# Kernel tuning notes

Hardware: AMD Instinct MI355X
Metric: run time of the kernel (lower is better)

The kernel has to match this reference:

```python
import jax, jax.numpy as jnp
import numpy as np

B, N, E = 2, 50000, 400000
C_IN, D, C, S, H, L, FFN = 5, 2, 128, 32, 8, 4, 512
COORD_F, TIME_F, FREQ_BASE, BETA = 8, 4, 1000.0, 1.0
HD = C // H


def setup_inputs() -> dict:
    key = jax.random.key(0)
    ks = jax.random.split(key, 32)
    sc = 0.02
    inp = {
        'inputs': jax.random.normal(ks[0], (B, N, C_IN), jnp.float32),
        'coords': jax.random.uniform(ks[1], (B, N, D), jnp.float32),
        't_norm': jax.random.uniform(ks[2], (B,), jnp.float32),
        'adj_indices': jax.random.randint(ks[3], (2, E), 0, N, jnp.int64 if jax.config.jax_enable_x64 else jnp.int32),
        'adj_values': jax.random.uniform(ks[4], (E,), jnp.float32) * 0.25,  # ~1/avg_degree for stable magnitudes
        'freq_matrix': jax.random.normal(ks[5], (D, COORD_F), jnp.float32),
        'embed_W': jax.random.normal(ks[6], (C_IN + 2 * COORD_F + 2 * TIME_F, C), jnp.float32) * sc,
        'embed_b': jnp.zeros((C,), jnp.float32),
        'ln1_g': jnp.ones((L, C), jnp.float32),
        'ln1_b': jnp.zeros((L, C), jnp.float32),
        'Wslice': jax.random.normal(ks[7], (L, C, S), jnp.float32) * sc,
        'bslice': jnp.zeros((L, S), jnp.float32),
        'Wfront': jax.random.normal(ks[8], (L, C, S), jnp.float32) * sc,
        'bfront': jnp.zeros((L, S), jnp.float32),
        'Win': jax.random.normal(ks[9], (L, C, 3 * C), jnp.float32) * sc,
        'b_in': jnp.zeros((L, 3 * C), jnp.float32),
        'Wout': jax.random.normal(ks[10], (L, C, C), jnp.float32) * sc,
        'bout': jnp.zeros((L, C), jnp.float32),
        'ln2_g': jnp.ones((L, C), jnp.float32),
        'ln2_b': jnp.zeros((L, C), jnp.float32),
        'Wff1': jax.random.normal(ks[11], (L, C, FFN), jnp.float32) * sc,
        'bff1': jnp.zeros((L, FFN), jnp.float32),
        'Wff2': jax.random.normal(ks[12], (L, FFN, C), jnp.float32) * sc,
        'bff2': jnp.zeros((L, C), jnp.float32),
        'proj_W': jax.random.normal(ks[13], (C, C_IN), jnp.float32) * sc,
        'proj_b': jnp.zeros((C_IN,), jnp.float32),
    }
    return inp


def _layer_norm(x, g, b, eps=1e-5):
    m = jnp.mean(x, -1, keepdims=True)
    v = jnp.mean(jnp.square(x - m), -1, keepdims=True)
    return (x - m) * jax.lax.rsqrt(v + eps) * g + b


def _forward(inputs, coords, t_norm, adj_indices, adj_values, freq_matrix,
             embed_W, embed_b, ln1_g, ln1_b, Wslice, bslice, Wfront, bfront,
             Win, b_in, Wout, bout, ln2_g, ln2_b, Wff1, bff1, Wff2, bff2,
             proj_W, proj_b):
    rows, cols = adj_indices[0], adj_indices[1]
    b, n = coords.shape[0], coords.shape[1]
    # spatial Fourier encoding (B,N,2*COORD_F)
    p = 2.0 * jnp.pi * (coords @ freq_matrix)
    sp_enc = jnp.concatenate([jnp.sin(p), jnp.cos(p)], -1)
    # temporal encoding (B,N,2*TIME_F)
    omega = FREQ_BASE ** (-jnp.arange(TIME_F, dtype=jnp.float32) / TIME_F)
    ang = omega[None, :] * (t_norm * FREQ_BASE)[:, None]
    t_enc = jnp.broadcast_to(jnp.concatenate([jnp.sin(ang), jnp.cos(ang)], -1)[:, None, :], (b, n, 2 * TIME_F))
    x = jnp.concatenate([inputs, sp_enc, t_enc], -1) @ embed_W + embed_b  # (B,N,C)
    weights_all = []
    for l in range(L):
        h = _layer_norm(x, ln1_g[l], ln1_b[l])
        # sparse adjacency aggregation: y[r] += a_e * h[c] (duplicates sum == coalesce)
        contrib = adj_values[None, :, None] * h[:, cols, :]  # (B,E,C)
        h_local = jax.vmap(lambda cb: jax.ops.segment_sum(cb, rows, num_segments=n))(contrib)
        h_front = h - h_local
        logits = h @ Wslice[l] + bslice[l] + BETA * (h_front @ Wfront[l] + bfront[l])
        w = jax.nn.softmax(logits, -1)  # (B,N,S)
        wsum = jnp.maximum(jnp.sum(w, axis=1)[:, :, None], 1e-8)  # (B,S,1)
        slices = jnp.einsum('bns,bnc->bsc', w, h) / wsum  # (B,S,C)
        # slice-space MHA (self-attention on S tokens)
        qkv = slices @ Win[l] + b_in[l]
        q, k, v = jnp.split(qkv, 3, axis=-1)
        def split_heads(t):
            return t.reshape(b, S, H, HD).transpose(0, 2, 1, 3)  # (B,H,S,HD)
        qh, kh, vh = split_heads(q), split_heads(k), split_heads(v)
        attn = jax.nn.softmax(jnp.einsum('bhqd,bhkd->bhqk', qh, kh) / jnp.sqrt(jnp.float32(HD)), -1)
        o = jnp.einsum('bhqk,bhkd->bhqd', attn, vh).transpose(0, 2, 1, 3).reshape(b, S, C)
        slices_out = o @ Wout[l] + bout[l]
        x = x + jnp.einsum('bns,bsc->bnc', w, slices_out)
        h2 = _layer_norm(x, ln2_g[l], ln2_b[l])
        x = x + jax.nn.gelu(h2 @ Wff1[l] + bff1[l], approximate=False) @ Wff2[l] + bff2[l]
        weights_all.append(w)
    out = x @ proj_W + proj_b  # (B,N,C_OUT)
    return out, jnp.stack(weights_all)  # (L,B,N,S)


def reference(inputs, coords, t_norm, adj_indices, adj_values, freq_matrix,
              embed_W, embed_b, ln1_g, ln1_b, Wslice, bslice, Wfront, bfront,
              Win, b_in, Wout, bout, ln2_g, ln2_b, Wff1, bff1, Wff2, bff2,
              proj_W, proj_b):
    return _forward(inputs, coords, t_norm, adj_indices, adj_values, freq_matrix,
                    embed_W, embed_b, ln1_g, ln1_b, Wslice, bslice, Wfront, bfront,
                    Win, b_in, Wout, bout, ln2_g, ln2_b, Wff1, bff1, Wff2, bff2,
                    proj_W, proj_b)
```

## Files before the change

kernel.cpp:

```cpp
#include <hip/hip_runtime.h>
#include <math.h>

#define BATCH 2
#define NN 50000
#define NE 400000
#define C_IN 5
#define CC 128
#define SS 32
#define NH 8
#define NL 4
#define FFN 512
#define COORD_F 8
#define TIME_F 4
#define HD 16
#define BETA 1.0f
#define TWO_PI 6.283185307179586476925287f

#define NTOT (BATCH * NN)
#define FF_MT 128
#define FF_BLOCKS ((NTOT + FF_MT - 1) / FF_MT)
#define MPAD (FF_BLOCKS * FF_MT)
#define NBLK ((NN + 127) / 128)
#define LP_PAD 136
#define H2S 136
#define HIDS 72

typedef unsigned short u16;
typedef unsigned int u32;
typedef __attribute__((ext_vector_type(8))) __bf16 bf16x8;
typedef __attribute__((ext_vector_type(4))) float f32x4;

__device__ __forceinline__ u16 f2bf(float f) {
    union { __bf16 b; u16 u; } v;
    v.b = (__bf16)f;
    return v.u;
}

__device__ __forceinline__ float bf2f(u16 h) {
    union { u32 u; float f; } v; v.u = ((u32)h) << 16;
    return v.f;
}

__device__ __forceinline__ float gelu_f(float a) {
    float xx = a * 0.7071067811865475f;
    float ax = fabsf(xx);
    float t = 1.0f / fmaf(0.3275911f, ax, 1.0f);
    float poly = t * fmaf(t, fmaf(t, fmaf(t, fmaf(t, 1.061405429f, -1.453152027f),
                                          1.421413741f), -0.284496736f), 0.254829592f);
    float e = __expf(-ax * ax);
    float erfv = copysignf(fmaf(-poly, e, 1.0f), xx);
    return 0.5f * a * (1.0f + erfv);
}

__global__ void count_deg(const int* rows, int* deg) {
    int e = blockIdx.x * blockDim.x + threadIdx.x;
    if (e < NE) atomicAdd(&deg[rows[e]], 1);
}

__global__ __launch_bounds__(512) void scan_deg(const int* deg, int* rowptr) {
    __shared__ int part[512];
    int t = threadIdx.x;
    const int CH = (NN + 511) / 512;
    int begin = t * CH, end = min(begin + CH, NN);
    int s = 0;
    for (int i = begin; i < end; i++) s += deg[i];
    part[t] = s;
    __syncthreads();
    for (int off = 1; off < 512; off <<= 1) {
        int v = (t >= off) ? part[t - off] : 0;
        __syncthreads();
        part[t] += v;
        __syncthreads();
    }
    int base = (t == 0) ? 0 : part[t - 1];
    for (int i = begin; i < end; i++) { rowptr[i] = base; base += deg[i]; }
    if (t == 511) rowptr[NN] = part[511];
}

__global__ void fill_csr(const int* rows, const int* cols, const float* vals,
                         int* cursor, int* csr_col, float* csr_val) {
    int e = blockIdx.x * blockDim.x + threadIdx.x;
    if (e < NE) {
        int p = atomicAdd(&cursor[rows[e]], 1);
        csr_col[p] = cols[e];
        csr_val[p] = vals[e];
    }
}

__global__ __launch_bounds__(128) void embed_ln1_kernel(const float* inputs, const float* coords,
                                                        const float* t_norm, const float* freq,
                                                        const float* W, const float* bias,
                                                        const float* g, const float* bb,
                                                        float* x, u16* hbf) {
    int node = blockIdx.x;
    int b = node / NN;
    int t = threadIdx.x;
    __shared__ float feat[32];
    __shared__ float sm[4];
    if (t < 8) {
        float c0 = coords[node * 2 + 0], c1 = coords[node * 2 + 1];
        float p = TWO_PI * (c0 * freq[t] + c1 * freq[8 + t]);
        feat[5 + t] = sinf(p);
        feat[13 + t] = cosf(p);
    } else if (t < 12) {
        int j = t - 8;
        float omega = powf(1000.0f, -(float)j * 0.25f);
        float ang = omega * t_norm[b] * 1000.0f;
        feat[21 + j] = sinf(ang);
        feat[25 + j] = cosf(ang);
    } else if (t >= 16 && t < 21) {
        feat[t - 16] = inputs[node * 5 + (t - 16)];
    }
    __syncthreads();
    float acc = bias[t];
    #pragma unroll
    for (int k = 0; k < 29; k++) acc += feat[k] * W[k * CC + t];
    x[(size_t)node * CC + t] = acc;
    float s = acc;
    #pragma unroll
    for (int off = 32; off > 0; off >>= 1) s += __shfl_xor(s, off, 64);
    if ((t & 63) == 0) sm[t >> 6] = s;
    __syncthreads();
    float mean = (sm[0] + sm[1]) * (1.0f / 128.0f);
    float d = acc - mean;
    float ss = d * d;
    #pragma unroll
    for (int off = 32; off > 0; off >>= 1) ss += __shfl_xor(ss, off, 64);
    if ((t & 63) == 0) sm[2 + (t >> 6)] = ss;
    __syncthreads();
    float var = (sm[2] + sm[3]) * (1.0f / 128.0f);
    hbf[(size_t)node * CC + t] = f2bf(d * rsqrtf(var + 1e-5f) * g[t] + bb[t]);
}

__global__ __launch_bounds__(128) void agg_kernel(const u16* hbf, const int* rowptr,
                                                  const int* csr_col, const float* csr_val,
                                                  u16* hlbf) {
    int blk = blockIdx.x;
    int b = blk / NN, r = blk % NN;
    int t = threadIdx.x;
    int s0 = rowptr[r], s1 = rowptr[r + 1];
    const u16* hb = hbf + (size_t)b * NN * CC;
    float a0 = 0.0f, a1 = 0.0f, a2 = 0.0f, a3 = 0.0f;
    int e = s0;
    for (; e + 4 <= s1; e += 4) {
        int c0 = csr_col[e], c1 = csr_col[e + 1], c2 = csr_col[e + 2], c3 = csr_col[e + 3];
        float v0 = csr_val[e], v1 = csr_val[e + 1], v2 = csr_val[e + 2], v3 = csr_val[e + 3];
        u16 h0 = hb[(size_t)c0 * CC + t];
        u16 h1 = hb[(size_t)c1 * CC + t];
        u16 h2 = hb[(size_t)c2 * CC + t];
        u16 h3 = hb[(size_t)c3 * CC + t];
        a0 += v0 * bf2f(h0);
        a1 += v1 * bf2f(h1);
        a2 += v2 * bf2f(h2);
        a3 += v3 * bf2f(h3);
    }
    for (; e < s1; e++) a0 += csr_val[e] * bf2f(hb[(size_t)csr_col[e] * CC + t]);
    hlbf[(size_t)blk * CC + t] = f2bf((a0 + a1) + (a2 + a3));
}

__global__ __launch_bounds__(256) void pack_logits_weights(const float* Ws, const float* bs,
                                                           const float* Wf, const float* bf,
                                                           u16* Wcombp, float* bcombp) {
    int idx = blockIdx.x * 256 + threadIdx.x;
    if (idx >= NL * SS * 256) return;
    int l = idx / (SS * 256);
    int r = idx - l * (SS * 256);
    int s = r >> 8, k = r & 255;
    float v;
    if (k < 128)
        v = Ws[(size_t)l * CC * SS + (size_t)k * SS + s] + BETA * Wf[(size_t)l * CC * SS + (size_t)k * SS + s];
    else
        v = -BETA * Wf[(size_t)l * CC * SS + (size_t)(k - 128) * SS + s];
    Wcombp[idx] = f2bf(v);
    if (k == 0) bcombp[l * SS + s] = bs[l * SS + s] + BETA * bf[l * SS + s];
}

__global__ __launch_bounds__(256, 2) void logits_pool(const u16* __restrict__ hbf,
                                                      const u16* __restrict__ hlbf,
                                                      const u16* __restrict__ Wcomb,
                                                      const float* __restrict__ bcomb,
                                                      float* __restrict__ wout,
                                                      u16* __restrict__ whi,
                                                      u16* __restrict__ wlo,
                                                      float* __restrict__ slices_acc,
                                                      float* __restrict__ wsum) {
    __shared__ __align__(16) u16 hT[128 * LP_PAD];
    __shared__ __align__(16) u16 wTh[SS * LP_PAD];
    __shared__ __align__(16) u16 wTl[SS * LP_PAD];
    __shared__ float wsum_sh[SS];
    int t = threadIdx.x;
    int b = blockIdx.y;
    int nl0 = blockIdx.x * 128;
    int wv = t >> 6, lane = t & 63;
    int q = lane >> 4, ln16 = lane & 15;
    int nl0w = nl0 + wv * 32;
    if (t < SS) wsum_sh[t] = 0.0f;
    __syncthreads();

    f32x4 acc[2][2];
    #pragma unroll
    for (int mi = 0; mi < 2; mi++)
        #pragma unroll
        for (int ni = 0; ni < 2; ni++) acc[mi][ni] = (f32x4){0.f, 0.f, 0.f, 0.f};

    #pragma unroll
    for (int ks = 0; ks < 8; ks++) {
        const u16* src = (ks < 4) ? hbf : hlbf;
        int ko = (ks & 3) * 32 + q * 8;
        bf16x8 af[2], bfrg[2];
        #pragma unroll
        for (int mi = 0; mi < 2; mi++) {
            int nl = nl0w + mi * 16 + ln16;
            af[mi] = *(const bf16x8*)&src[((size_t)b * NN + nl) * CC + ko];
            if (ks < 4) {
                bool valid = nl < NN;
                const u16* ap = (const u16*)&af[mi];
                int nlb = nl - nl0;
                #pragma unroll
                for (int i = 0; i < 8; i++)
                    hT[(ko + i) * LP_PAD + nlb] = valid ? ap[i] : (u16)0;
            }
        }
        #pragma unroll
        for (int ni = 0; ni < 2; ni++)
            bfrg[ni] = *(const bf16x8*)&Wcomb[(size_t)(ni * 16 + ln16) * 256 + ks * 32 + q * 8];
        #pragma unroll
        for (int mi = 0; mi < 2; mi++)
            #pragma unroll
            for (int ni = 0; ni < 2; ni++)
                acc[mi][ni] = __builtin_amdgcn_mfma_f32_16x16x32_bf16(af[mi], bfrg[ni], acc[mi][ni], 0, 0, 0);
    }

    float bc0 = bcomb[ln16], bc1 = bcomb[16 + ln16];
    float ws0 = 0.0f, ws1 = 0.0f;
    #pragma unroll
    for (int mi = 0; mi < 2; mi++)
        #pragma unroll
        for (int r = 0; r < 4; r++) {
            float l0 = acc[mi][0][r] + bc0;
            float l1 = acc[mi][1][r] + bc1;
            float m = fmaxf(l0, l1);
            #pragma unroll
            for (int msk = 1; msk < 16; msk <<= 1) m = fmaxf(m, __shfl_xor(m, msk, 64));
            float e0 = __expf(l0 - m), e1 = __expf(l1 - m);
            float sum = e0 + e1;
            #pragma unroll
            for (int msk = 1; msk < 16; msk <<= 1) sum += __shfl_xor(sum, msk, 64);
            float is = 1.0f / sum;
            int nl = nl0w + mi * 16 + q * 4 + r;
            bool valid = nl < NN;
            float w0 = valid ? e0 * is : 0.0f;
            float w1 = valid ? e1 * is : 0.0f;
            u16 h0 = f2bf(w0), h1 = f2bf(w1);
            u16 lo0 = f2bf(w0 - bf2f(h0)), lo1 = f2bf(w1 - bf2f(h1));
            if (valid) {
                size_t gb = ((size_t)b * NN + nl) * SS;
                wout[gb + ln16] = w0;
                wout[gb + 16 + ln16] = w1;
                whi[gb + ln16] = h0;  wlo[gb + ln16] = lo0;
                whi[gb + 16 + ln16] = h1;  wlo[gb + 16 + ln16] = lo1;
            }
            int nlb = nl - nl0;
            wTh[ln16 * LP_PAD + nlb] = h0;  wTl[ln16 * LP_PAD + nlb] = lo0;
            wTh[(16 + ln16) * LP_PAD + nlb] = h1;  wTl[(16 + ln16) * LP_PAD + nlb] = lo1;
            ws0 += w0;  ws1 += w1;
        }
    ws0 += __shfl_xor(ws0, 16, 64); ws0 += __shfl_xor(ws0, 32, 64);
    ws1 += __shfl_xor(ws1, 16, 64); ws1 += __shfl_xor(ws1, 32, 64);
    if (q == 0) {
        atomicAdd(&wsum_sh[ln16], ws0);
        atomicAdd(&wsum_sh[16 + ln16], ws1);
    }
    __syncthreads();

    f32x4 pacc[2][8];
    #pragma unroll
    for (int st = 0; st < 2; st++)
        #pragma unroll
        for (int ct = 0; ct < 8; ct++) pacc[st][ct] = (f32x4){0.f, 0.f, 0.f, 0.f};
    {
        int kb = wv * 32 + q * 8;
        bf16x8 wh[2], wl2[2];
        #pragma unroll
        for (int st = 0; st < 2; st++) {
            wh[st] = *(const bf16x8*)&wTh[(st * 16 + ln16) * LP_PAD + kb];
            wl2[st] = *(const bf16x8*)&wTl[(st * 16 + ln16) * LP_PAD + kb];
        }
        #pragma unroll
        for (int ct = 0; ct < 8; ct++) {
            bf16x8 bfr = *(const bf16x8*)&hT[(ct * 16 + ln16) * LP_PAD + kb];
            #pragma unroll
            for (int st = 0; st < 2; st++) {
                pacc[st][ct] = __builtin_amdgcn_mfma_f32_16x16x32_bf16(wh[st], bfr, pacc[st][ct], 0, 0, 0);
                pacc[st][ct] = __builtin_amdgcn_mfma_f32_16x16x32_bf16(wl2[st], bfr, pacc[st][ct], 0, 0, 0);
            }
        }
    }
    __syncthreads();

    float* red = (float*)hT;
    for (int i = t; i < SS * CC; i += 256) red[i] = 0.0f;
    __syncthreads();
    #pragma unroll
    for (int st = 0; st < 2; st++)
        #pragma unroll
        for (int ct = 0; ct < 8; ct++)
            #pragma unroll
            for (int r = 0; r < 4; r++)
                atomicAdd(&red[(st * 16 + q * 4 + r) * CC + ct * 16 + ln16], pacc[st][ct][r]);
    __syncthreads();
    if (t < SS) atomicAdd(&wsum[b * SS + t], wsum_sh[t]);
    #pragma unroll
    for (int k = 0; k < 16; k++) {
        int idx = k * 256 + t;
        atomicAdd(&slices_acc[(size_t)b * SS * CC + idx], red[idx]);
    }
}

__global__ __launch_bounds__(128) void qkv_kernel(const float* slices_acc, const float* wsum,
                                                  const float* Win, const float* b_in_p,
                                                  float* qkv) {
    int blk = blockIdx.x;
    int t = threadIdx.x;
    __shared__ float row[128];
    float iv = 1.0f / fmaxf(wsum[blk], 1e-8f);
    row[t] = slices_acc[(size_t)blk * CC + t] * iv;
    __syncthreads();
    #pragma unroll
    for (int jj = 0; jj < 3; jj++) {
        int j = t + jj * 128;
        float a = b_in_p[j];
        #pragma unroll 8
        for (int c = 0; c < 128; c++) a += row[c] * Win[c * 384 + j];
        qkv[(size_t)blk * 384 + j] = a;
    }
}

__global__ __launch_bounds__(64) void attn_kernel(const float* qkv, float* ovals) {
    int blk = blockIdx.x;
    int b = blk >> 3, h = blk & 7;
    int t = threadIdx.x;
    __shared__ float ksh[32 * 16], vsh[32 * 16];
    for (int i = t; i < 512; i += 64) {
        int k = i >> 4, d = i & 15;
        ksh[i] = qkv[((size_t)b * 32 + k) * 384 + 128 + h * 16 + d];
        vsh[i] = qkv[((size_t)b * 32 + k) * 384 + 256 + h * 16 + d];
    }
    __syncthreads();
    if (t < 32) {
        float qr[16];
        #pragma unroll
        for (int d = 0; d < 16; d++) qr[d] = qkv[((size_t)b * 32 + t) * 384 + h * 16 + d];
        float sc[32];
        float m = -1e30f;
        for (int k = 0; k < 32; k++) {
            float a = 0.0f;
            #pragma unroll
            for (int d = 0; d < 16; d++) a += qr[d] * ksh[k * 16 + d];
            a *= 0.25f;
            sc[k] = a;
            m = fmaxf(m, a);
        }
        float ssum = 0.0f;
        for (int k = 0; k < 32; k++) { float e = expf(sc[k] - m); sc[k] = e; ssum += e; }
        float is = 1.0f / ssum;
        float o[16];
        #pragma unroll
        for (int d = 0; d < 16; d++) o[d] = 0.0f;
        for (int k = 0; k < 32; k++) {
            float p = sc[k] * is;
            #pragma unroll
            for (int d = 0; d < 16; d++) o[d] += p * vsh[k * 16 + d];
        }
        #pragma unroll
        for (int d = 0; d < 16; d++) ovals[((size_t)b * 32 + t) * 128 + h * 16 + d] = o[d];
    }
}

__global__ __launch_bounds__(128) void mha_out_kernel(const float* ovals, const float* Wout,
                                                      const float* bout,
                                                      u16* soThi, u16* soTlo) {
    int blk = blockIdx.x;
    int b = blk >> 5, s = blk & 31;
    int t = threadIdx.x;
    __shared__ float row[128];
    row[t] = ovals[(size_t)blk * 128 + t];
    __syncthreads();
    float a = bout[t];
    #pragma unroll 8
    for (int cc = 0; cc < 128; cc++) a += row[cc] * Wout[cc * CC + t];
    u16 hi = f2bf(a);
    size_t idx = (size_t)b * CC * SS + (size_t)t * SS + s;
    soThi[idx] = hi;
    soTlo[idx] = f2bf(a - bf2f(hi));
}

__global__ __launch_bounds__(256) void pack_ffn_weights(const float* Wff1, const float* Wff2,
                                                        u16* W1p, u16* W2p) {
    int idx = blockIdx.x * 256 + threadIdx.x;
    if (idx >= NL * FFN * CC) return;
    int l = idx / (FFN * CC);
    int r = idx - l * (FFN * CC);
    int j = r >> 7, c = r & 127;
    W1p[idx] = f2bf(Wff1[(size_t)l * CC * FFN + (size_t)c * FFN + j]);
    int c2 = r >> 9, j2 = r & 511;
    W2p[idx] = f2bf(Wff2[(size_t)l * FFN * CC + (size_t)j2 * CC + c2]);
}

__global__ __launch_bounds__(256, 2) void ffn_mega(float* __restrict__ x,
                                                   const u16* __restrict__ whi,
                                                   const u16* __restrict__ wlo,
                                                   const u16* __restrict__ soThi,
                                                   const u16* __restrict__ soTlo,
                                                   const float* __restrict__ g,
                                                   const float* __restrict__ bb,
                                                   const u16* __restrict__ W1p,
                                                   const float* __restrict__ bff1,
                                                   const u16* __restrict__ W2p,
                                                   const float* __restrict__ bff2,
                                                   const float* __restrict__ g1,
                                                   const float* __restrict__ b1,
                                                   u16* __restrict__ hbf_out) {
    __shared__ __align__(16) u16 smem[128 * 144];
    __shared__ __align__(16) float rowst[128 * 4];
    u16* h2t = smem;
    int t = threadIdx.x;
    int b = blockIdx.y;
    int n0 = blockIdx.x * 128;
    int wave = t >> 6, lane = t & 63;
    int wm = wave >> 1, wn = wave & 1;
    int q = lane >> 4, ln16 = lane & 15;
    bool emit = (g1 != nullptr);

    float gr[4], br[4];
    #pragma unroll
    for (int ni = 0; ni < 4; ni++) {
        int col = wn * 64 + ni * 16 + ln16;
        gr[ni] = g[col]; br[ni] = bb[col];
    }

    f32x4 acc2[4][4];
    #pragma unroll
    for (int mi = 0; mi < 4; mi++)
        #pragma unroll
        for (int ni = 0; ni < 4; ni++) acc2[mi][ni] = (f32x4){0.f, 0.f, 0.f, 0.f};

    {
        const u16* soh = soThi + (size_t)b * CC * SS;
        const u16* sol = soTlo + (size_t)b * CC * SS;
        bf16x8 bh[4], bl[4], ah[4], al[4];
        bf16x8 zf;
        #pragma unroll
        for (int i = 0; i < 8; i++) zf[i] = (__bf16)0.0f;
        #pragma unroll
        for (int ni = 0; ni < 4; ni++) {
            int c = wn * 64 + ni * 16 + ln16;
            bh[ni] = *(const bf16x8*)&soh[c * SS + q * 8];
            bl[ni] = *(const bf16x8*)&sol[c * SS + q * 8];
        }
        #pragma unroll
        for (int mi = 0; mi < 4; mi++) {
            int row = n0 + wm * 64 + mi * 16 + ln16;
            if (row < NN) {
                size_t base = ((size_t)b * NN + row) * SS + q * 8;
                ah[mi] = *(const bf16x8*)&whi[base];
                al[mi] = *(const bf16x8*)&wlo[base];
            } else { ah[mi] = zf; al[mi] = zf; }
        }
        #pragma unroll
        for (int mi = 0; mi < 4; mi++)
            #pragma unroll
            for (int ni = 0; ni < 4; ni++) {
                acc2[mi][ni] = __builtin_amdgcn_mfma_f32_16x16x32_bf16(ah[mi], bh[ni], acc2[mi][ni], 0, 0, 0);
                acc2[mi][ni] = __builtin_amdgcn_mfma_f32_16x16x32_bf16(al[mi], bh[ni], acc2[mi][ni], 0, 0, 0);
                acc2[mi][ni] = __builtin_amdgcn_mfma_f32_16x16x32_bf16(ah[mi], bl[ni], acc2[mi][ni], 0, 0, 0);
            }
    }

    #pragma unroll
    for (int mi = 0; mi < 4; mi++)
        #pragma unroll
        for (int r = 0; r < 4; r++) {
            int row = n0 + wm * 64 + mi * 16 + q * 4 + r;
            if (row < NN) {
                const float* xr = &x[((size_t)b * NN + row) * CC + wn * 64 + ln16];
                #pragma unroll
                for (int ni = 0; ni < 4; ni++) acc2[mi][ni][r] += xr[ni * 16];
            }
        }
    #pragma unroll
    for (int mi = 0; mi < 4; mi++)
        #pragma unroll
        for (int r = 0; r < 4; r++) {
            float a = acc2[mi][0][r] + acc2[mi][1][r] + acc2[mi][2][r] + acc2[mi][3][r];
            float a2 = acc2[mi][0][r] * acc2[mi][0][r] + acc2[mi][1][r] * acc2[mi][1][r] +
                       acc2[mi][2][r] * acc2[mi][2][r] + acc2[mi][3][r] * acc2[mi][3][r];
            #pragma unroll
            for (int msk = 1; msk < 16; msk <<= 1) {
                a += __shfl_xor(a, msk, 64);
                a2 += __shfl_xor(a2, msk, 64);
            }
            if (ln16 == 0) {
                int m = wm * 64 + mi * 16 + q * 4 + r;
                rowst[m * 4 + wn * 2] = a;
                rowst[m * 4 + wn * 2 + 1] = a2;
            }
        }
    __syncthreads();
    #pragma unroll
    for (int mi = 0; mi < 4; mi++)
        #pragma unroll
        for (int r = 0; r < 4; r++) {
            int m = wm * 64 + mi * 16 + q * 4 + r;
            float s1 = rowst[m * 4 + 0] + rowst[m * 4 + 2];
            float s2 = rowst[m * 4 + 1] + rowst[m * 4 + 3];
            float mean = s1 * (1.0f / 128.0f);
            float var = s2 * (1.0f / 128.0f) - mean * mean;
            float rstd = rsqrtf(fmaxf(var, 0.0f) + 1e-5f);
            #pragma unroll
            for (int ni = 0; ni < 4; ni++) {
                int col = wn * 64 + ni * 16 + ln16;
                h2t[m * H2S + col] = f2bf((acc2[mi][ni][r] - mean) * rstd * gr[ni] + br[ni]);
            }
        }
    __syncthreads();

    bf16x8 areg[4][4];
    #pragma unroll
    for (int ks = 0; ks < 4; ks++)
        #pragma unroll
        for (int mi = 0; mi < 4; mi++)
            areg[ks][mi] = *(const bf16x8*)&h2t[(wm * 64 + mi * 16 + ln16) * H2S + ks * 32 + q * 8];
    __syncthreads();

    for (int jc = 0; jc < 8; jc++) {
        u16* hid = smem + (jc & 1) * (128 * HIDS);
        f32x4 acc1[4][2];
        #pragma unroll
        for (int mi = 0; mi < 4; mi++)
            #pragma unroll
            for (int ni = 0; ni < 2; ni++) acc1[mi][ni] = (f32x4){0.f, 0.f, 0.f, 0.f};

        __builtin_amdgcn_s_setprio(1);
        #pragma unroll
        for (int ks = 0; ks < 4; ks++) {
            bf16x8 bfr[2];
            #pragma unroll
            for (int ni = 0; ni < 2; ni++)
                bfr[ni] = *(const bf16x8*)&W1p[(size_t)(jc * 64 + wn * 32 + ni * 16 + ln16) * CC + ks * 32 + q * 8];
            #pragma unroll
            for (int mi = 0; mi < 4; mi++)
                #pragma unroll
                for (int ni = 0; ni < 2; ni++)
                    acc1[mi][ni] = __builtin_amdgcn_mfma_f32_16x16x32_bf16(areg[ks][mi], bfr[ni], acc1[mi][ni], 0, 0, 0);
        }
        __builtin_amdgcn_s_setprio(0);

        #pragma unroll
        for (int ni = 0; ni < 2; ni++) {
            float b1v = bff1[jc * 64 + wn * 32 + ni * 16 + ln16];
            #pragma unroll
            for (int mi = 0; mi < 4; mi++)
                #pragma unroll
                for (int r = 0; r < 4; r++)
                    hid[(wm * 64 + mi * 16 + q * 4 + r) * HIDS + wn * 32 + ni * 16 + ln16] =
                        f2bf(gelu_f(acc1[mi][ni][r] + b1v));
        }
        __syncthreads();

        __builtin_amdgcn_s_setprio(1);
        #pragma unroll
        for (int ks2 = 0; ks2 < 2; ks2++) {
            bf16x8 af[4], bfr[4];
            #pragma unroll
            for (int mi = 0; mi < 4; mi++)
                af[mi] = *(const bf16x8*)&hid[(wm * 64 + mi * 16 + ln16) * HIDS + ks2 * 32 + q * 8];
            #pragma unroll
            for (int ni = 0; ni < 4; ni++)
                bfr[ni] = *(const bf16x8*)&W2p[(size_t)(wn * 64 + ni * 16 + ln16) * FFN + jc * 64 + ks2 * 32 + q * 8];
            #pragma unroll
            for (int mi = 0; mi < 4; mi++)
                #pragma unroll
                for (int ni = 0; ni < 4; ni++)
                    acc2[mi][ni] = __builtin_amdgcn_mfma_f32_16x16x32_bf16(af[mi], bfr[ni], acc2[mi][ni], 0, 0, 0);
        }
        __builtin_amdgcn_s_setprio(0);
    }

    float b2[4];
    #pragma unroll
    for (int ni = 0; ni < 4; ni++) b2[ni] = bff2[wn * 64 + ni * 16 + ln16];
    #pragma unroll
    for (int mi = 0; mi < 4; mi++)
        #pragma unroll
        for (int ni = 0; ni < 4; ni++)
            #pragma unroll
            for (int r = 0; r < 4; r++) acc2[mi][ni][r] += b2[ni];

    #pragma unroll
    for (int mi = 0; mi < 4; mi++)
        #pragma unroll
        for (int r = 0; r < 4; r++) {
            int row = n0 + wm * 64 + mi * 16 + q * 4 + r;
            if (row < NN) {
                float* xo = &x[((size_t)b * NN + row) * CC + wn * 64 + ln16];
                #pragma unroll
                for (int ni = 0; ni < 4; ni++) xo[ni * 16] = acc2[mi][ni][r];
            }
        }

    if (emit) {
        float g1r[4], b1r[4];
        #pragma unroll
        for (int ni = 0; ni < 4; ni++) {
            int col = wn * 64 + ni * 16 + ln16;
            g1r[ni] = g1[col]; b1r[ni] = b1[col];
        }
        #pragma unroll
        for (int mi = 0; mi < 4; mi++)
            #pragma unroll
            for (int r = 0; r < 4; r++) {
                float a = acc2[mi][0][r] + acc2[mi][1][r] + acc2[mi][2][r] + acc2[mi][3][r];
                float a2 = acc2[mi][0][r] * acc2[mi][0][r] + acc2[mi][1][r] * acc2[mi][1][r] +
                           acc2[mi][2][r] * acc2[mi][2][r] + acc2[mi][3][r] * acc2[mi][3][r];
                #pragma unroll
                for (int msk = 1; msk < 16; msk <<= 1) {
                    a += __shfl_xor(a, msk, 64);
                    a2 += __shfl_xor(a2, msk, 64);
                }
                if (ln16 == 0) {
                    int m = wm * 64 + mi * 16 + q * 4 + r;
                    rowst[m * 4 + wn * 2] = a;
                    rowst[m * 4 + wn * 2 + 1] = a2;
                }
            }
        __syncthreads();
        #pragma unroll
        for (int mi = 0; mi < 4; mi++)
            #pragma unroll
            for (int r = 0; r < 4; r++) {
                int m = wm * 64 + mi * 16 + q * 4 + r;
                float s1 = rowst[m * 4 + 0] + rowst[m * 4 + 2];
                float s2 = rowst[m * 4 + 1] + rowst[m * 4 + 3];
                float mean = s1 * (1.0f / 128.0f);
                float var = s2 * (1.0f / 128.0f) - mean * mean;
                float rstd = rsqrtf(fmaxf(var, 0.0f) + 1e-5f);
                #pragma unroll
                for (int ni = 0; ni < 4; ni++) {
                    int col = wn * 64 + ni * 16 + ln16;
                    smem[m * H2S + col] = f2bf((acc2[mi][ni][r] - mean) * rstd * g1r[ni] + b1r[ni]);
                }
            }
        __syncthreads();
        #pragma unroll
        for (int it = 0; it < 8; it++) {
            int chunk = it * 256 + t;
            int m = chunk >> 4;
            int c8 = (chunk & 15) << 3;
            int row = n0 + m;
            if (row < NN)
                *(f32x4*)&hbf_out[((size_t)b * NN + row) * CC + c8] =
                    *(const f32x4*)&smem[m * H2S + c8];
        }
    }
}

__global__ __launch_bounds__(128) void proj_kernel(const float* x, const float* W,
                                                   const float* bias, float* outp) {
    int node = blockIdx.x;
    int t = threadIdx.x;
    __shared__ float xr[128];
    __shared__ float pr[40];
    xr[t] = x[(size_t)node * CC + t];
    __syncthreads();
    if (t < 40) {
        int k = t / 8, part = t % 8;
        float a = 0.0f;
        #pragma unroll
        for (int i = 0; i < 16; i++) {
            int c = part * 16 + i;
            a += xr[c] * W[c * C_IN + k];
        }
        pr[t] = a;
    }
    __syncthreads();
    if (t < 5) {
        float a = bias[t];
        #pragma unroll
        for (int p = 0; p < 8; p++) a += pr[t * 8 + p];
        outp[(size_t)node * C_IN + t] = a;
    }
}

extern "C" void kernel_launch(void* const* d_in, const int* in_sizes, int n_in,
                              void* d_out, int out_size, void* d_ws, size_t ws_size,
                              hipStream_t stream) {
    const float* inputs  = (const float*)d_in[0];
    const float* coords  = (const float*)d_in[1];
    const float* t_norm  = (const float*)d_in[2];
    const int*   adj     = (const int*)d_in[3];
    const float* adj_v   = (const float*)d_in[4];
    const float* freq    = (const float*)d_in[5];
    const float* embed_W = (const float*)d_in[6];
    const float* embed_b = (const float*)d_in[7];
    const float* ln1_g   = (const float*)d_in[8];
    const float* ln1_b   = (const float*)d_in[9];
    const float* Wslice  = (const float*)d_in[10];
    const float* bslice  = (const float*)d_in[11];
    const float* Wfront  = (const float*)d_in[12];
    const float* bfront  = (const float*)d_in[13];
    const float* Win     = (const float*)d_in[14];
    const float* b_in    = (const float*)d_in[15];
    const float* Wout    = (const float*)d_in[16];
    const float* bout    = (const float*)d_in[17];
    const float* ln2_g   = (const float*)d_in[18];
    const float* ln2_b   = (const float*)d_in[19];
    const float* Wff1    = (const float*)d_in[20];
    const float* bff1    = (const float*)d_in[21];
    const float* Wff2    = (const float*)d_in[22];
    const float* bff2    = (const float*)d_in[23];
    const float* proj_W  = (const float*)d_in[24];
    const float* proj_b  = (const float*)d_in[25];

    float* out = (float*)d_out;
    float* wout_base = out + (size_t)BATCH * NN * C_IN;

    float* x          = (float*)d_ws;
    u16*   hbf        = (u16*)(x + (size_t)NTOT * CC);
    u16*   hlbf       = hbf + (size_t)MPAD * CC;
    u16*   whi        = hlbf + (size_t)MPAD * CC;
    u16*   wlo        = whi + (size_t)(NTOT + 128) * SS;
    u16*   soThi      = wlo + (size_t)(NTOT + 128) * SS;
    u16*   soTlo      = soThi + BATCH * CC * SS;
    float* slices_acc = (float*)(soTlo + BATCH * CC * SS);
    float* wsum       = slices_acc + BATCH * SS * CC;
    float* qkv_ws     = wsum + BATCH * SS;
    float* ovals_ws   = qkv_ws + BATCH * SS * 384;
    float* csr_val    = ovals_ws + BATCH * SS * CC;
    int*   rowptr     = (int*)(csr_val + NE);
    int*   cursor     = rowptr + (NN + 1);
    int*   deg        = cursor + NN;
    int*   csr_col    = deg + NN;
    u16*   W1p        = (u16*)(csr_col + NE);
    u16*   W2p        = W1p + NL * FFN * CC;
    u16*   Wcombp     = W2p + NL * CC * FFN;
    float* bcomb      = (float*)(Wcombp + NL * SS * 256);

    hipMemsetAsync(deg, 0, NN * sizeof(int), stream);
    count_deg<<<(NE + 255) / 256, 256, 0, stream>>>(adj, deg);
    scan_deg<<<1, 512, 0, stream>>>(deg, rowptr);
    hipMemcpyAsync(cursor, rowptr, NN * sizeof(int), hipMemcpyDeviceToDevice, stream);
    fill_csr<<<(NE + 255) / 256, 256, 0, stream>>>(adj, adj + NE, adj_v, cursor, csr_col, csr_val);

    pack_ffn_weights<<<(NL * FFN * CC + 255) / 256, 256, 0, stream>>>(Wff1, Wff2, W1p, W2p);
    pack_logits_weights<<<(NL * SS * 256 + 255) / 256, 256, 0, stream>>>(Wslice, bslice, Wfront,
                                                                         bfront, Wcombp, bcomb);

    embed_ln1_kernel<<<NTOT, 128, 0, stream>>>(inputs, coords, t_norm, freq, embed_W, embed_b,
                                               ln1_g, ln1_b, x, hbf);

    for (int l = 0; l < NL; l++) {
        float* wl = wout_base + (size_t)l * NTOT * SS;
        agg_kernel<<<NTOT, 128, 0, stream>>>(hbf, rowptr, csr_col, csr_val, hlbf);
        hipMemsetAsync(slices_acc, 0, (BATCH * SS * CC + BATCH * SS) * sizeof(float), stream);
        dim3 glp(NBLK, BATCH);
        logits_pool<<<glp, 256, 0, stream>>>(hbf, hlbf, Wcombp + (size_t)l * SS * 256,
                                             bcomb + l * SS, wl, whi, wlo, slices_acc, wsum);
        qkv_kernel<<<BATCH * SS, 128, 0, stream>>>(slices_acc, wsum,
                                                   Win + (size_t)l * CC * 3 * CC,
                                                   b_in + l * 3 * CC, qkv_ws);
        attn_kernel<<<BATCH * NH, 64, 0, stream>>>(qkv_ws, ovals_ws);
        mha_out_kernel<<<BATCH * SS, 128, 0, stream>>>(ovals_ws, Wout + (size_t)l * CC * CC,
                                                       bout + l * CC, soThi, soTlo);
        const float* g1n = (l + 1 < NL) ? (ln1_g + (size_t)(l + 1) * CC) : nullptr;
        const float* b1n = (l + 1 < NL) ? (ln1_b + (size_t)(l + 1) * CC) : nullptr;
        dim3 g3(NBLK, BATCH);
        ffn_mega<<<g3, 256, 0, stream>>>(x, whi, wlo, soThi, soTlo,
                                         ln2_g + l * CC, ln2_b + l * CC,
                                         W1p + (size_t)l * FFN * CC, bff1 + l * FFN,
                                         W2p + (size_t)l * CC * FFN, bff2 + l * CC,
                                         g1n, b1n, hbf);
    }

    proj_kernel<<<NTOT, 128, 0, stream>>>(x, proj_W, proj_b, out);
}
```

Measured before the change: 1.815 ms.

## Split FFN mega-kernel tile across 8 waves to cut per-wave registers

Launches the fused FFN kernel with 512 threads (8 waves) per 128-row tile instead of 256, so each wave owns 32 rows rather than 64. This halves the per-wave accumulator and A-fragment register footprint, targeting more resident waves per CU to hide latency. The residual x rows are also prefetched before the first MFMAs, and the W2 fragments for the first k-slice are loaded before the GELU/store phase to overlap global loads with compute. The cost is that W1/W2 fragments are now reloaded by twice as many waves and there is more barrier traffic per tile.

```diff
diff --git a/kernel.cpp b/kernel.cpp
--- a/kernel.cpp
+++ b/kernel.cpp
@@ -407,7 +407,7 @@
     W2p[idx] = f2bf(Wff2[(size_t)l * FFN * CC + (size_t)j2 * CC + c2]);
 }
 
-__global__ __launch_bounds__(256, 2) void ffn_mega(float* __restrict__ x,
+__global__ __launch_bounds__(512, 4) void ffn_mega(float* __restrict__ x,
                                                    const u16* __restrict__ whi,
                                                    const u16* __restrict__ wlo,
                                                    const u16* __restrict__ soThi,
@@ -439,16 +439,18 @@
         gr[ni] = g[col]; br[ni] = bb[col];
     }
 
-    f32x4 acc2[4][4];
-    #pragma unroll
-    for (int mi = 0; mi < 4; mi++)
+    f32x4 acc2[2][4];
+    #pragma unroll
+    for (int mi = 0; mi < 2; mi++)
         #pragma unroll
         for (int ni = 0; ni < 4; ni++) acc2[mi][ni] = (f32x4){0.f, 0.f, 0.f, 0.f};
+
+    float xr[2][4][4];
 
     {
         const u16* soh = soThi + (size_t)b * CC * SS;
         const u16* sol = soTlo + (size_t)b * CC * SS;
-        bf16x8 bh[4], bl[4], ah[4], al[4];
+        bf16x8 bh[4], bl[4], ah[2], al[2];
         bf16x8 zf;
         #pragma unroll
         for (int i = 0; i < 8; i++) zf[i] = (__bf16)0.0f;
@@ -459,8 +461,8 @@
             bl[ni] = *(const bf16x8*)&sol[c * SS + q * 8];
         }
         #pragma unroll
-        for (int mi = 0; mi < 4; mi++) {
-            int row = n0 + wm * 64 + mi * 16 + ln16;
+        for (int mi = 0; mi < 2; mi++) {
+            int row = n0 + wm * 32 + mi * 16 + ln16;
             if (row < NN) {
                 size_t base = ((size_t)b * NN + row) * SS + q * 8;
                 ah[mi] = *(const bf16x8*)&whi[base];
@@ -468,28 +470,35 @@
             } else { ah[mi] = zf; al[mi] = zf; }
         }
         #pragma unroll
-        for (int mi = 0; mi < 4; mi++)
+        for (int mi = 0; mi < 2; mi++)
+            #pragma unroll
+            for (int r = 0; r < 4; r++) {
+                int row = n0 + wm * 32 + mi * 16 + q * 4 + r;
+                bool v = row < NN;
+                const float* xp = &x[((size_t)b * NN + row) * CC + wn * 64 + ln16];
+                #pragma unroll
+                for (int ni = 0; ni < 4; ni++) xr[mi][r][ni] = v ? xp[ni * 16] : 0.0f;
+            }
+        __builtin_amdgcn_s_setprio(1);
+        #pragma unroll
+        for (int mi = 0; mi < 2; mi++)
             #pragma unroll
             for (int ni = 0; ni < 4; ni++) {
                 acc2[mi][ni] = __builtin_amdgcn_mfma_f32_16x16x32_bf16(ah[mi], bh[ni], acc2[mi][ni], 0, 0, 0);
                 acc2[mi][ni] = __builtin_amdgcn_mfma_f32_16x16x32_bf16(al[mi], bh[ni], acc2[mi][ni], 0, 0, 0);
                 acc2[mi][ni] = __builtin_amdgcn_mfma_f32_16x16x32_bf16(ah[mi], bl[ni], acc2[mi][ni], 0, 0, 0);
             }
-    }
-
-    #pragma unroll
-    for (int mi = 0; mi < 4; mi++)
-        #pragma unroll
-        for (int r = 0; r < 4; r++) {
-            int row = n0 + wm * 64 + mi * 16 + q * 4 + r;
-            if (row < NN) {
-                const float* xr = &x[((size_t)b * NN + row) * CC + wn * 64 + ln16];
-                #pragma unroll
-                for (int ni = 0; ni < 4; ni++) acc2[mi][ni][r] += xr[ni * 16];
-            }
-        }
-    #pragma unroll
-    for (int mi = 0; mi < 4; mi++)
+        __builtin_amdgcn_s_setprio(0);
+    }
+
+    #pragma unroll
+    for (int mi = 0; mi < 2; mi++)
+        #pragma unroll
+        for (int r = 0; r < 4; r++)
+            #pragma unroll
+            for (int ni = 0; ni < 4; ni++) acc2[mi][ni][r] += xr[mi][r][ni];
+    #pragma unroll
+    for (int mi = 0; mi < 2; mi++)
         #pragma unroll
         for (int r = 0; r < 4; r++) {
             float a = acc2[mi][0][r] + acc2[mi][1][r] + acc2[mi][2][r] + acc2[mi][3][r];
@@ -501,17 +510,17 @@
                 a2 += __shfl_xor(a2, msk, 64);
             }
             if (ln16 == 0) {
-                int m = wm * 64 + mi * 16 + q * 4 + r;
+                int m = wm * 32 + mi * 16 + q * 4 + r;
                 rowst[m * 4 + wn * 2] = a;
                 rowst[m * 4 + wn * 2 + 1] = a2;
             }
         }
     __syncthreads();
     #pragma unroll
-    for (int mi = 0; mi < 4; mi++)
+    for (int mi = 0; mi < 2; mi++)
         #pragma unroll
         for (int r = 0; r < 4; r++) {
-            int m = wm * 64 + mi * 16 + q * 4 + r;
+            int m = wm * 32 + mi * 16 + q * 4 + r;
             float s1 = rowst[m * 4 + 0] + rowst[m * 4 + 2];
             float s2 = rowst[m * 4 + 1] + rowst[m * 4 + 3];
             float mean = s1 * (1.0f / 128.0f);
@@ -525,19 +534,19 @@
         }
     __syncthreads();
 
-    bf16x8 areg[4][4];
+    bf16x8 areg[4][2];
     #pragma unroll
     for (int ks = 0; ks < 4; ks++)
         #pragma unroll
-        for (int mi = 0; mi < 4; mi++)
-            areg[ks][mi] = *(const bf16x8*)&h2t[(wm * 64 + mi * 16 + ln16) * H2S + ks * 32 + q * 8];
+        for (int mi = 0; mi < 2; mi++)
+            areg[ks][mi] = *(const bf16x8*)&h2t[(wm * 32 + mi * 16 + ln16) * H2S + ks * 32 + q * 8];
     __syncthreads();
 
     for (int jc = 0; jc < 8; jc++) {
         u16* hid = smem + (jc & 1) * (128 * HIDS);
-        f32x4 acc1[4][2];
-        #pragma unroll
-        for (int mi = 0; mi < 4; mi++)
+        f32x4 acc1[2][2];
+        #pragma unroll
+        for (int mi = 0; mi < 2; mi++)
             #pragma unroll
             for (int ni = 0; ni < 2; ni++) acc1[mi][ni] = (f32x4){0.f, 0.f, 0.f, 0.f};
 
@@ -549,40 +558,53 @@
             for (int ni = 0; ni < 2; ni++)
                 bfr[ni] = *(const bf16x8*)&W1p[(size_t)(jc * 64 + wn * 32 + ni * 16 + ln16) * CC + ks * 32 + q * 8];
             #pragma unroll
-            for (int mi = 0; mi < 4; mi++)
+            for (int mi = 0; mi < 2; mi++)
                 #pragma unroll
                 for (int ni = 0; ni < 2; ni++)
                     acc1[mi][ni] = __builtin_amdgcn_mfma_f32_16x16x32_bf16(areg[ks][mi], bfr[ni], acc1[mi][ni], 0, 0, 0);
         }
         __builtin_amdgcn_s_setprio(0);
 
+        bf16x8 b2f0[4];
+        #pragma unroll
+        for (int ni = 0; ni < 4; ni++)
+            b2f0[ni] = *(const bf16x8*)&W2p[(size_t)(wn * 64 + ni * 16 + ln16) * FFN + jc * 64 + q * 8];
+
         #pragma unroll
         for (int ni = 0; ni < 2; ni++) {
             float b1v = bff1[jc * 64 + wn * 32 + ni * 16 + ln16];
             #pragma unroll
-            for (int mi = 0; mi < 4; mi++)
+            for (int mi = 0; mi < 2; mi++)
                 #pragma unroll
                 for (int r = 0; r < 4; r++)
-                    hid[(wm * 64 + mi * 16 + q * 4 + r) * HIDS + wn * 32 + ni * 16 + ln16] =
+                    hid[(wm * 32 + mi * 16 + q * 4 + r) * HIDS + wn * 32 + ni * 16 + ln16] =
                         f2bf(gelu_f(acc1[mi][ni][r] + b1v));
         }
         __syncthreads();
 
         __builtin_amdgcn_s_setprio(1);
-        #pragma unroll
-        for (int ks2 = 0; ks2 < 2; ks2++) {
-            bf16x8 af[4], bfr[4];
-            #pragma unroll
-            for (int mi = 0; mi < 4; mi++)
-                af[mi] = *(const bf16x8*)&hid[(wm * 64 + mi * 16 + ln16) * HIDS + ks2 * 32 + q * 8];
-            #pragma unroll
-            for (int ni = 0; ni < 4; ni++)
-                bfr[ni] = *(const bf16x8*)&W2p[(size_t)(wn * 64 + ni * 16 + ln16) * FFN + jc * 64 + ks2 * 32 + q * 8];
-            #pragma unroll
-            for (int mi = 0; mi < 4; mi++)
+        {
+            bf16x8 af0[2];
+            #pragma unroll
+            for (int mi = 0; mi < 2; mi++)
+                af0[mi] = *(const bf16x8*)&hid[(wm * 32 + mi * 16 + ln16) * HIDS + q * 8];
+            #pragma unroll
+            for (int mi = 0; mi < 2; mi++)
                 #pragma unroll
                 for (int ni = 0; ni < 4; ni++)
-                    acc2[mi][ni] = __builtin_amdgcn_mfma_f32_16x16x32_bf16(af[mi], bfr[ni], acc2[mi][ni], 0, 0, 0);
+                    acc2[mi][ni] = __builtin_amdgcn_mfma_f32_16x16x32_bf16(af0[mi], b2f0[ni], acc2[mi][ni], 0, 0, 0);
+            bf16x8 af1[2], b2f1[4];
+            #pragma unroll
+            for (int mi = 0; mi < 2; mi++)
+                af1[mi] = *(const bf16x8*)&hid[(wm * 32 + mi * 16 + ln16) * HIDS + 32 + q * 8];
+            #pragma unroll
+            for (int ni = 0; ni < 4; ni++)
+                b2f1[ni] = *(const bf16x8*)&W2p[(size_t)(wn * 64 + ni * 16 + ln16) * FFN + jc * 64 + 32 + q * 8];
+            #pragma unroll
+            for (int mi = 0; mi < 2; mi++)
+                #pragma unroll
+                for (int ni = 0; ni < 4; ni++)
+                    acc2[mi][ni] = __builtin_amdgcn_mfma_f32_16x16x32_bf16(af1[mi], b2f1[ni], acc2[mi][ni], 0, 0, 0);
         }
         __builtin_amdgcn_s_setprio(0);
     }
@@ -591,17 +613,17 @@
     #pragma unroll
     for (int ni = 0; ni < 4; ni++) b2[ni] = bff2[wn * 64 + ni * 16 + ln16];
     #pragma unroll
-    for (int mi = 0; mi < 4; mi++)
+    for (int mi = 0; mi < 2; mi++)
         #pragma unroll
         for (int ni = 0; ni < 4; ni++)
             #pragma unroll
             for (int r = 0; r < 4; r++) acc2[mi][ni][r] += b2[ni];
 
     #pragma unroll
-    for (int mi = 0; mi < 4; mi++)
+    for (int mi = 0; mi < 2; mi++)
         #pragma unroll
         for (int r = 0; r < 4; r++) {
-            int row = n0 + wm * 64 + mi * 16 + q * 4 + r;
+            int row = n0 + wm * 32 + mi * 16 + q * 4 + r;
             if (row < NN) {
                 float* xo = &x[((size_t)b * NN + row) * CC + wn * 64 + ln16];
                 #pragma unroll
@@ -617,7 +639,7 @@
             g1r[ni] = g1[col]; b1r[ni] = b1[col];
         }
         #pragma unroll
-        for (int mi = 0; mi < 4; mi++)
+        for (int mi = 0; mi < 2; mi++)
             #pragma unroll
             for (int r = 0; r < 4; r++) {
                 float a = acc2[mi][0][r] + acc2[mi][1][r] + acc2[mi][2][r] + acc2[mi][3][r];
@@ -629,17 +651,17 @@
                     a2 += __shfl_xor(a2, msk, 64);
                 }
                 if (ln16 == 0) {
-                    int m = wm * 64 + mi * 16 + q * 4 + r;
+                    int m = wm * 32 + mi * 16 + q * 4 + r;
                     rowst[m * 4 + wn * 2] = a;
                     rowst[m * 4 + wn * 2 + 1] = a2;
                 }
             }
         __syncthreads();
         #pragma unroll
-        for (int mi = 0; mi < 4; mi++)
+        for (int mi = 0; mi < 2; mi++)
             #pragma unroll
             for (int r = 0; r < 4; r++) {
-                int m = wm * 64 + mi * 16 + q * 4 + r;
+                int m = wm * 32 + mi * 16 + q * 4 + r;
                 float s1 = rowst[m * 4 + 0] + rowst[m * 4 + 2];
                 float s2 = rowst[m * 4 + 1] + rowst[m * 4 + 3];
                 float mean = s1 * (1.0f / 128.0f);
@@ -653,8 +675,8 @@
             }
         __syncthreads();
         #pragma unroll
-        for (int it = 0; it < 8; it++) {
-            int chunk = it * 256 + t;
+        for (int it = 0; it < 4; it++) {
+            int chunk = it * 512 + t;
             int m = chunk >> 4;
             int c8 = (chunk & 15) << 3;
             int row = n0 + m;
@@ -775,7 +797,7 @@
         const float* g1n = (l + 1 < NL) ? (ln1_g + (size_t)(l + 1) * CC) : nullptr;
         const float* b1n = (l + 1 < NL) ? (ln1_b + (size_t)(l + 1) * CC) : nullptr;
         dim3 g3(NBLK, BATCH);
-        ffn_mega<<<g3, 256, 0, stream>>>(x, whi, wlo, soThi, soTlo,
+        ffn_mega<<<g3, 512, 0, stream>>>(x, whi, wlo, soThi, soTlo,
                                          ln2_g + l * CC, ln2_b + l * CC,
                                          W1p + (size_t)l * FFN * CC, bff1 + l * FFN,
                                          W2p + (size_t)l * CC * FFN, bff2 + l * CC,
```

Result: slower. 2.014 ms (+11.0%).
